# Kernel optimization log

Measured on AMD Instinct MI355X. Metric: run time of the kernel, lower is better.

The kernel has to match this reference:

```python
import jax, jax.numpy as jnp
import numpy as np

N_NODES = 100000
IN_CH = 64
HID = 128
N_EDGES = 1600000


def sage_conv(x, src, dst, Wl, bl, Wr, num_nodes):
    # PyG SAGEConv (mean aggr): out = lin_l(mean_{j->i} x_j) + lin_r(x_i)
    msg = x[src]                                           # [E, F] gather
    agg = jax.ops.segment_sum(msg, dst, num_segments=num_nodes)   # [N, F]
    cnt = jax.ops.segment_sum(jnp.ones((src.shape[0],), x.dtype), dst,
                              num_segments=num_nodes)      # [N]
    mean = agg / jnp.maximum(cnt, 1.0)[:, None]
    return mean @ Wl.T + bl + x @ Wr.T


def setup_inputs() -> dict:
    key = jax.random.key(0)
    k1, k2, k3, k4, k5, k6, k7, k8 = jax.random.split(key, 8)
    x = jax.random.normal(k1, (N_NODES, IN_CH), dtype=jnp.float32)
    edge_index = jax.random.randint(k2, (2, N_EDGES), 0, N_NODES, dtype=jnp.int64)
    s1 = 1.0 / np.sqrt(IN_CH)
    s2 = 1.0 / np.sqrt(HID)
    Wl1 = jax.random.uniform(k3, (HID, IN_CH), jnp.float32, -s1, s1)
    bl1 = jax.random.uniform(k4, (HID,), jnp.float32, -s1, s1)
    Wr1 = jax.random.uniform(k5, (HID, IN_CH), jnp.float32, -s1, s1)
    Wl2 = jax.random.uniform(k6, (HID, HID), jnp.float32, -s2, s2)
    bl2 = jax.random.uniform(k7, (HID,), jnp.float32, -s2, s2)
    Wr2 = jax.random.uniform(k8, (HID, HID), jnp.float32, -s2, s2)
    return {"x": x, "edge_index": edge_index,
            "Wl1": Wl1, "bl1": bl1, "Wr1": Wr1,
            "Wl2": Wl2, "bl2": bl2, "Wr2": Wr2}


def reference(x, edge_index, Wl1, bl1, Wr1, Wl2, bl2, Wr2):
    src, dst = edge_index[0], edge_index[1]
    n = x.shape[0]
    h = sage_conv(x, src, dst, Wl1, bl1, Wr1, n)
    h = jax.nn.relu(h)
    # dropout p=0.2 is identity in eval/reference mode
    out = sage_conv(h, src, dst, Wl2, bl2, Wr2, n)
    return out
```

## Files before the change

### kernel.cpp

```cpp
#include <hip/hip_runtime.h>
#include <hip/hip_bf16.h>
#include <stdint.h>

#define NN 100000
#define EE 1600000
#define NBUCK 196
#define CSB 512

typedef __attribute__((ext_vector_type(4))) float f32x4;
typedef __attribute__((ext_vector_type(8))) short bf16x8;

__device__ inline ushort f2bf(float f) {
    union { float f; uint32_t u; } v; v.f = f;
    uint32_t u = v.u;
    uint32_t r = (u + 0x7fffu + ((u >> 16) & 1u)) >> 16;
    return (ushort)r;
}
__device__ inline float bflo(uint32_t u) {
    union { uint32_t u; float f; } v; v.u = u << 16; return v.f;
}
__device__ inline float bfhi(uint32_t u) {
    union { uint32_t u; float f; } v; v.u = u & 0xffff0000u; return v.f;
}

__global__ void detect_kernel(const unsigned int* raw, int* flag) {
    int i = blockIdx.x * blockDim.x + threadIdx.x;
    if (i < 4096) {
        if (raw[2 * i + 1] != 0u) atomicOr(flag, 1);
    }
}

__global__ void cvt_f32_bf16(const float* __restrict__ in, ushort* __restrict__ out, int n4) {
    int i = blockIdx.x * blockDim.x + threadIdx.x;
    if (i >= n4) return;
    float4 v = *(const float4*)&in[i * 4];
    ushort o[4] = { f2bf(v.x), f2bf(v.y), f2bf(v.z), f2bf(v.w) };
    *(uint64_t*)&out[i * 4] = *(const uint64_t*)o;
}

__global__ void build_wcat(const float* __restrict__ Wl, const float* __restrict__ Wr,
                           ushort* __restrict__ Wcat, int K) {
    int t = blockIdx.x * blockDim.x + threadIdx.x;
    int KT = 2 * K;
    if (t >= 128 * KT) return;
    int o = t / KT, k = t % KT;
    float v = (k < K) ? Wl[o * K + k] : Wr[o * K + (k - K)];
    Wcat[o * KT + k] = f2bf(v);
}

__global__ __launch_bounds__(256) void coarse_hist(const void* raw, const int* flag,
                                                   int* ccnt, int E) {
    __shared__ int lh[NBUCK];
    for (int i = threadIdx.x; i < NBUCK; i += 256) lh[i] = 0;
    __syncthreads();
    int stride = gridDim.x * 256;
    if (*flag) {
        const int* p = (const int*)raw;
        for (int e = blockIdx.x * 256 + threadIdx.x; e < E; e += stride)
            atomicAdd(&lh[p[E + e] >> 9], 1);
    } else {
        const long long* p = (const long long*)raw;
        for (int e = blockIdx.x * 256 + threadIdx.x; e < E; e += stride)
            atomicAdd(&lh[((int)p[E + e]) >> 9], 1);
    }
    __syncthreads();
    for (int i = threadIdx.x; i < NBUCK; i += 256)
        if (lh[i]) atomicAdd(&ccnt[i], lh[i]);
}

__global__ void coarse_scan(const int* ccnt, int* coff, int* offsets, int E) {
    __shared__ int part[256];
    int t = threadIdx.x;
    int v[4]; int s = 0;
    #pragma unroll
    for (int j = 0; j < 4; j++) {
        int i = t * 4 + j;
        v[j] = (i < NBUCK) ? ccnt[i] : 0;
        s += v[j];
    }
    part[t] = s; __syncthreads();
    for (int off = 1; off < 256; off <<= 1) {
        int add = (t >= off) ? part[t - off] : 0;
        __syncthreads();
        part[t] += add;
        __syncthreads();
    }
    int run = part[t] - s;
    #pragma unroll
    for (int j = 0; j < 4; j++) {
        int i = t * 4 + j;
        if (i <= NBUCK) coff[i] = run;
        run += v[j];
    }
    if (t == 0) offsets[NN] = E;
}

__global__ __launch_bounds__(256) void coarse_scatter2(const void* raw, const int* flag,
                                                       const int* coff, int* cfill,
                                                       uint32_t* pbuf, int E) {
    __shared__ int lh[NBUCK];
    __shared__ int gbase[NBUCK];
    __shared__ int lfill[NBUCK];
    const int t = threadIdx.x;
    for (int i = t; i < NBUCK; i += 256) { lh[i] = 0; lfill[i] = 0; }
    __syncthreads();
    const int chunk = (E + (int)gridDim.x - 1) / (int)gridDim.x;
    const int s0 = blockIdx.x * chunk;
    const int s1 = min(E, s0 + chunk);
    const bool is32 = (*flag != 0);
    if (is32) {
        const int* p = (const int*)raw;
        for (int e = s0 + t; e < s1; e += 256) atomicAdd(&lh[p[E + e] >> 9], 1);
    } else {
        const long long* p = (const long long*)raw;
        for (int e = s0 + t; e < s1; e += 256) atomicAdd(&lh[((int)p[E + e]) >> 9], 1);
    }
    __syncthreads();
    for (int i = t; i < NBUCK; i += 256)
        gbase[i] = coff[i] + (lh[i] ? atomicAdd(&cfill[i], lh[i]) : 0);
    __syncthreads();
    if (is32) {
        const int* p = (const int*)raw;
        for (int e = s0 + t; e < s1; e += 256) {
            int sr = p[e], d = p[E + e];
            int b = d >> 9;
            int r = atomicAdd(&lfill[b], 1);
            pbuf[gbase[b] + r] = ((uint32_t)(d & 511) << 17) | (uint32_t)sr;
        }
    } else {
        const long long* p = (const long long*)raw;
        for (int e = s0 + t; e < s1; e += 256) {
            int sr = (int)p[e], d = (int)p[E + e];
            int b = d >> 9;
            int r = atomicAdd(&lfill[b], 1);
            pbuf[gbase[b] + r] = ((uint32_t)(d & 511) << 17) | (uint32_t)sr;
        }
    }
}

__global__ __launch_bounds__(512) void fine_bucket(const uint32_t* __restrict__ pbuf,
                                                   const int* __restrict__ coff,
                                                   int* __restrict__ offsets,
                                                   int* __restrict__ srcs_sort, int N) {
    __shared__ int cnt[512], sc[512], fil[512];
    const int b = blockIdx.x, t = threadIdx.x;
    const int s = coff[b], e = coff[b + 1];
    cnt[t] = 0; fil[t] = 0;
    __syncthreads();
    for (int i = s + t; i < e; i += 512) atomicAdd(&cnt[pbuf[i] >> 17], 1);
    __syncthreads();
    sc[t] = cnt[t];
    __syncthreads();
    for (int off = 1; off < 512; off <<= 1) {
        int add = (t >= off) ? sc[t - off] : 0;
        __syncthreads();
        sc[t] += add;
        __syncthreads();
    }
    const int nb0 = b * 512;
    if (nb0 + t < N) offsets[nb0 + t] = s + sc[t] - cnt[t];
    for (int i = s + t; i < e; i += 512) {
        uint32_t p = pbuf[i];
        int dl = (int)(p >> 17);
        int sr = (int)(p & 0x1FFFFu);
        int pos = s + (sc[dl] - cnt[dl]) + atomicAdd(&fil[dl], 1);
        srcs_sort[pos] = sr;
    }
}

template<int K, bool RELU, bool OUT_BF16>
__global__ __launch_bounds__(256) void sage_fused(
    const int* __restrict__ offsets, const int* __restrict__ srcs,
    const ushort* __restrict__ xin, const ushort* __restrict__ Wcat,
    const float* __restrict__ bl, void* __restrict__ outv, int N)
{
    constexpr int KT = 2 * K;
    constexpr int RP = K + 8;
    __shared__ ushort mlds[32][RP];
    __shared__ ushort slds[32][RP];
    const int t = threadIdx.x;
    const int w = t >> 6;
    const int lane = t & 63;
    const int nb = blockIdx.x * 32;

    #pragma unroll
    for (int idx = t; idx < 32 * (K / 8); idx += 256) {
        int r = idx / (K / 8), c = idx % (K / 8);
        *(uint4*)&slds[r][c * 8] = *(const uint4*)&xin[(size_t)(nb + r) * K + c * 8];
    }

    const int q     = lane >> 4;
    const int ql    = lane & 15;
    const int qbase = lane & 48;

    int offv = 0;
    if (lane < 9) offv = offsets[nb + w * 8 + lane];

    for (int pi = 0; pi < 2; pi++) {
        const int ln = w * 8 + pi * 4 + q;
        const int s0 = __shfl(offv, pi * 4 + q);
        const int s1 = __shfl(offv, pi * 4 + q + 1);
        const float inv = 1.0f / fmaxf((float)(s1 - s0), 1.0f);

        if (K == 64) {
            float f0=0.f, f1=0.f, f2=0.f, f3=0.f;
            for (int base = s0; base < s1; base += 16) {
                int cnt = min(16, s1 - base);
                int myidx = (base + ql < s1) ? srcs[base + ql] : 0;
                int j = 0;
                for (; j + 4 <= cnt; j += 4) {
                    int sA = __shfl(myidx, qbase + j);
                    int sB = __shfl(myidx, qbase + j + 1);
                    int sC = __shfl(myidx, qbase + j + 2);
                    int sD = __shfl(myidx, qbase + j + 3);
                    uint2 uA = *(const uint2*)&xin[(size_t)sA * 64 + ql * 4];
                    uint2 uB = *(const uint2*)&xin[(size_t)sB * 64 + ql * 4];
                    uint2 uC = *(const uint2*)&xin[(size_t)sC * 64 + ql * 4];
                    uint2 uD = *(const uint2*)&xin[(size_t)sD * 64 + ql * 4];
                    f0 += bflo(uA.x); f1 += bfhi(uA.x); f2 += bflo(uA.y); f3 += bfhi(uA.y);
                    f0 += bflo(uB.x); f1 += bfhi(uB.x); f2 += bflo(uB.y); f3 += bfhi(uB.y);
                    f0 += bflo(uC.x); f1 += bfhi(uC.x); f2 += bflo(uC.y); f3 += bfhi(uC.y);
                    f0 += bflo(uD.x); f1 += bfhi(uD.x); f2 += bflo(uD.y); f3 += bfhi(uD.y);
                }
                for (; j < cnt; j++) {
                    int s = __shfl(myidx, qbase + j);
                    uint2 u = *(const uint2*)&xin[(size_t)s * 64 + ql * 4];
                    f0 += bflo(u.x); f1 += bfhi(u.x); f2 += bflo(u.y); f3 += bfhi(u.y);
                }
            }
            ushort o[4] = { f2bf(f0 * inv), f2bf(f1 * inv), f2bf(f2 * inv), f2bf(f3 * inv) };
            *(uint64_t*)&mlds[ln][ql * 4] = *(const uint64_t*)o;
        } else {
            float f0=0.f, f1=0.f, f2=0.f, f3=0.f, f4=0.f, f5=0.f, f6=0.f, f7=0.f;
            for (int base = s0; base < s1; base += 16) {
                int cnt = min(16, s1 - base);
                int myidx = (base + ql < s1) ? srcs[base + ql] : 0;
                int j = 0;
                for (; j + 4 <= cnt; j += 4) {
                    int sA = __shfl(myidx, qbase + j);
                    int sB = __shfl(myidx, qbase + j + 1);
                    int sC = __shfl(myidx, qbase + j + 2);
                    int sD = __shfl(myidx, qbase + j + 3);
                    uint4 uA = *(const uint4*)&xin[(size_t)sA * 128 + ql * 8];
                    uint4 uB = *(const uint4*)&xin[(size_t)sB * 128 + ql * 8];
                    uint4 uC = *(const uint4*)&xin[(size_t)sC * 128 + ql * 8];
                    uint4 uD = *(const uint4*)&xin[(size_t)sD * 128 + ql * 8];
                    f0 += bflo(uA.x); f1 += bfhi(uA.x); f2 += bflo(uA.y); f3 += bfhi(uA.y);
                    f4 += bflo(uA.z); f5 += bfhi(uA.z); f6 += bflo(uA.w); f7 += bfhi(uA.w);
                    f0 += bflo(uB.x); f1 += bfhi(uB.x); f2 += bflo(uB.y); f3 += bfhi(uB.y);
                    f4 += bflo(uB.z); f5 += bfhi(uB.z); f6 += bflo(uB.w); f7 += bfhi(uB.w);
                    f0 += bflo(uC.x); f1 += bfhi(uC.x); f2 += bflo(uC.y); f3 += bfhi(uC.y);
                    f4 += bflo(uC.z); f5 += bfhi(uC.z); f6 += bflo(uC.w); f7 += bfhi(uC.w);
                    f0 += bflo(uD.x); f1 += bfhi(uD.x); f2 += bflo(uD.y); f3 += bfhi(uD.y);
                    f4 += bflo(uD.z); f5 += bfhi(uD.z); f6 += bflo(uD.w); f7 += bfhi(uD.w);
                }
                for (; j < cnt; j++) {
                    int s = __shfl(myidx, qbase + j);
                    uint4 u = *(const uint4*)&xin[(size_t)s * 128 + ql * 8];
                    f0 += bflo(u.x); f1 += bfhi(u.x); f2 += bflo(u.y); f3 += bfhi(u.y);
                    f4 += bflo(u.z); f5 += bfhi(u.z); f6 += bflo(u.w); f7 += bfhi(u.w);
                }
            }
            ushort o[8] = { f2bf(f0 * inv), f2bf(f1 * inv), f2bf(f2 * inv), f2bf(f3 * inv),
                            f2bf(f4 * inv), f2bf(f5 * inv), f2bf(f6 * inv), f2bf(f7 * inv) };
            *(uint4*)&mlds[ln][ql * 8] = *(const uint4*)o;
        }
    }
    __syncthreads();

    const int lrow = lane & 15;
    const int lgrp = lane >> 4;
    f32x4 acc[2][2];
    #pragma unroll
    for (int nt = 0; nt < 2; nt++)
        #pragma unroll
        for (int ct = 0; ct < 2; ct++)
            acc[nt][ct] = (f32x4){0.f, 0.f, 0.f, 0.f};

    #pragma unroll
    for (int ks = 0; ks < KT; ks += 32) {
        const int ac = (ks < K) ? ks : (ks - K);
        const ushort* Xb = (ks < K) ? &mlds[0][0] : &slds[0][0];
        bf16x8 x0 = *(const bf16x8*)&Xb[(lrow) * RP + ac + lgrp * 8];
        bf16x8 x1 = *(const bf16x8*)&Xb[(16 + lrow) * RP + ac + lgrp * 8];
        bf16x8 wA = *(const bf16x8*)&Wcat[(size_t)(w * 32 + lrow) * KT + ks + lgrp * 8];
        bf16x8 wB = *(const bf16x8*)&Wcat[(size_t)(w * 32 + 16 + lrow) * KT + ks + lgrp * 8];
        acc[0][0] = __builtin_amdgcn_mfma_f32_16x16x32_bf16(wA, x0, acc[0][0], 0, 0, 0);
        acc[0][1] = __builtin_amdgcn_mfma_f32_16x16x32_bf16(wB, x0, acc[0][1], 0, 0, 0);
        acc[1][0] = __builtin_amdgcn_mfma_f32_16x16x32_bf16(wA, x1, acc[1][0], 0, 0, 0);
        acc[1][1] = __builtin_amdgcn_mfma_f32_16x16x32_bf16(wB, x1, acc[1][1], 0, 0, 0);
    }

    #pragma unroll
    for (int ct = 0; ct < 2; ct++) {
        const int ch0 = w * 32 + ct * 16 + lgrp * 4;
        float4 b4 = *(const float4*)&bl[ch0];
        #pragma unroll
        for (int nt = 0; nt < 2; nt++) {
            int n = nb + nt * 16 + lrow;
            float v0 = acc[nt][ct][0] + b4.x;
            float v1 = acc[nt][ct][1] + b4.y;
            float v2 = acc[nt][ct][2] + b4.z;
            float v3 = acc[nt][ct][3] + b4.w;
            if (RELU) {
                v0 = fmaxf(v0, 0.f); v1 = fmaxf(v1, 0.f);
                v2 = fmaxf(v2, 0.f); v3 = fmaxf(v3, 0.f);
            }
            if (OUT_BF16) {
                ushort o[4] = { f2bf(v0), f2bf(v1), f2bf(v2), f2bf(v3) };
                *(uint64_t*)&((ushort*)outv)[(size_t)n * 128 + ch0] = *(const uint64_t*)o;
            } else {
                float4 o = make_float4(v0, v1, v2, v3);
                *(float4*)&((float*)outv)[(size_t)n * 128 + ch0] = o;
            }
        }
    }
}

extern "C" void kernel_launch(void* const* d_in, const int* in_sizes, int n_in,
                              void* d_out, int out_size, void* d_ws, size_t ws_size,
                              hipStream_t stream) {
    const float* x   = (const float*)d_in[0];
    const void*  er  = d_in[1];
    const float* Wl1 = (const float*)d_in[2];
    const float* bl1 = (const float*)d_in[3];
    const float* Wr1 = (const float*)d_in[4];
    const float* Wl2 = (const float*)d_in[5];
    const float* bl2 = (const float*)d_in[6];
    const float* Wr2 = (const float*)d_in[7];
    float* out = (float*)d_out;

    const int N = NN, E = EE;

    char* ws = (char*)d_ws;
    size_t off = 0;
    auto carve = [&](size_t bytes) { char* p = ws + off; off += (bytes + 511) & ~(size_t)511; return p; };
    int*      flag      = (int*)     carve(4);
    int*      ccnt      = (int*)     carve((size_t)NBUCK * 4);
    int*      cfill     = (int*)     carve((size_t)NBUCK * 4);
    int*      coff      = (int*)     carve((size_t)(NBUCK + 1) * 4);
    uint32_t* pbuf      = (uint32_t*)carve((size_t)E * 4);
    int*      offsets   = (int*)     carve((size_t)(N + 1) * 4);
    int*      srcs_sort = (int*)     carve((size_t)E * 4);
    ushort*   xb        = (ushort*)  carve((size_t)N * 64 * 2);
    ushort*   hb        = (ushort*)  carve((size_t)N * 128 * 2);
    ushort*   wc1       = (ushort*)  carve((size_t)128 * 128 * 2);
    ushort*   wc2       = (ushort*)  carve((size_t)128 * 256 * 2);
    (void)ws_size;

    hipMemsetAsync(flag, 0, 4, stream);
    hipMemsetAsync(ccnt, 0, (size_t)NBUCK * 4, stream);
    hipMemsetAsync(cfill, 0, (size_t)NBUCK * 4, stream);

    detect_kernel<<<16, 256, 0, stream>>>((const unsigned int*)er, flag);

    cvt_f32_bf16<<<(N * 64 / 4 + 255) / 256, 256, 0, stream>>>(x, xb, N * 64 / 4);
    build_wcat<<<(128 * 128 + 255) / 256, 256, 0, stream>>>(Wl1, Wr1, wc1, 64);
    build_wcat<<<(128 * 256 + 255) / 256, 256, 0, stream>>>(Wl2, Wr2, wc2, 128);

    coarse_hist<<<512, 256, 0, stream>>>(er, flag, ccnt, E);
    coarse_scan<<<1, 256, 0, stream>>>(ccnt, coff, offsets, E);
    coarse_scatter2<<<CSB, 256, 0, stream>>>(er, flag, coff, cfill, pbuf, E);
    fine_bucket<<<NBUCK, 512, 0, stream>>>(pbuf, coff, offsets, srcs_sort, N);

    const int fb = N / 32;

    sage_fused<64, true, true><<<fb, 256, 0, stream>>>(offsets, srcs_sort, xb, wc1, bl1, hb, N);
    sage_fused<128, false, false><<<fb, 256, 0, stream>>>(offsets, srcs_sort, hb, wc2, bl2, out, N);
}
```

Measured before the change: 210.5 us.

## Fuse prep kernels into one launch and sort each node's source list

Merges the detect, memset, x-to-bf16 conversion and two weight-concatenation kernels into one grid-stride prep kernel, cutting several launches and two memset calls. It also adds a per-node insertion sort of the source indices at the end of fine_bucket, so neighbor gathers in the sage kernels read x rows in increasing address order for better cache locality. The sort adds serial work per thread (about 16 edges per node) and the fused kernel relies on the flag memset finishing before it runs.

```diff
diff --git a/kernel.cpp b/kernel.cpp
--- a/kernel.cpp
+++ b/kernel.cpp
@@ -23,29 +23,38 @@
     union { uint32_t u; float f; } v; v.u = u & 0xffff0000u; return v.f;
 }
 
-__global__ void detect_kernel(const unsigned int* raw, int* flag) {
-    int i = blockIdx.x * blockDim.x + threadIdx.x;
-    if (i < 4096) {
-        if (raw[2 * i + 1] != 0u) atomicOr(flag, 1);
-    }
-}
-
-__global__ void cvt_f32_bf16(const float* __restrict__ in, ushort* __restrict__ out, int n4) {
-    int i = blockIdx.x * blockDim.x + threadIdx.x;
-    if (i >= n4) return;
-    float4 v = *(const float4*)&in[i * 4];
-    ushort o[4] = { f2bf(v.x), f2bf(v.y), f2bf(v.z), f2bf(v.w) };
-    *(uint64_t*)&out[i * 4] = *(const uint64_t*)o;
-}
-
-__global__ void build_wcat(const float* __restrict__ Wl, const float* __restrict__ Wr,
-                           ushort* __restrict__ Wcat, int K) {
-    int t = blockIdx.x * blockDim.x + threadIdx.x;
-    int KT = 2 * K;
-    if (t >= 128 * KT) return;
-    int o = t / KT, k = t % KT;
-    float v = (k < K) ? Wl[o * K + k] : Wr[o * K + (k - K)];
-    Wcat[o * KT + k] = f2bf(v);
+__global__ __launch_bounds__(256) void prep_kernel(
+    const float* __restrict__ x, const unsigned int* __restrict__ raw,
+    const float* __restrict__ Wl1, const float* __restrict__ Wr1,
+    const float* __restrict__ Wl2, const float* __restrict__ Wr2,
+    ushort* __restrict__ xb, ushort* __restrict__ wc1, ushort* __restrict__ wc2,
+    int* __restrict__ flag, int* __restrict__ ccnt, int* __restrict__ cfill)
+{
+    const int gid = blockIdx.x * 256 + threadIdx.x;
+    const int stride = gridDim.x * 256;
+
+    if (gid < 4096) {
+        if (raw[2 * gid + 1] != 0u) atomicOr(flag, 1);
+    }
+    if (gid >= 4096 && gid < 4096 + NBUCK) ccnt[gid - 4096] = 0;
+    if (gid >= 4096 + NBUCK && gid < 4096 + 2 * NBUCK) cfill[gid - 4096 - NBUCK] = 0;
+
+    const int n4 = NN * 64 / 4;
+    for (int i = gid; i < n4; i += stride) {
+        float4 v = *(const float4*)&x[i * 4];
+        ushort o[4] = { f2bf(v.x), f2bf(v.y), f2bf(v.z), f2bf(v.w) };
+        *(uint64_t*)&xb[i * 4] = *(const uint64_t*)o;
+    }
+    for (int i = gid; i < 128 * 128; i += stride) {
+        int o = i >> 7, k = i & 127;
+        float v = (k < 64) ? Wl1[o * 64 + k] : Wr1[o * 64 + (k - 64)];
+        wc1[o * 128 + k] = f2bf(v);
+    }
+    for (int i = gid; i < 128 * 256; i += stride) {
+        int o = i >> 8, k = i & 255;
+        float v = (k < 128) ? Wl2[o * 128 + k] : Wr2[o * 128 + (k - 128)];
+        wc2[o * 256 + k] = f2bf(v);
+    }
 }
 
 __global__ __launch_bounds__(256) void coarse_hist(const void* raw, const int* flag,
@@ -165,6 +174,17 @@
         int sr = (int)(p & 0x1FFFFu);
         int pos = s + (sc[dl] - cnt[dl]) + atomicAdd(&fil[dl], 1);
         srcs_sort[pos] = sr;
+    }
+    __syncthreads();
+    {
+        int a  = s + sc[t] - cnt[t];
+        int e2 = a + cnt[t];
+        for (int i = a + 1; i < e2; i++) {
+            int v = srcs_sort[i];
+            int j = i - 1;
+            while (j >= a && srcs_sort[j] > v) { srcs_sort[j + 1] = srcs_sort[j]; j--; }
+            srcs_sort[j + 1] = v;
+        }
     }
 }
 
@@ -349,14 +369,10 @@
     (void)ws_size;
 
     hipMemsetAsync(flag, 0, 4, stream);
-    hipMemsetAsync(ccnt, 0, (size_t)NBUCK * 4, stream);
-    hipMemsetAsync(cfill, 0, (size_t)NBUCK * 4, stream);
-
-    detect_kernel<<<16, 256, 0, stream>>>((const unsigned int*)er, flag);
-
-    cvt_f32_bf16<<<(N * 64 / 4 + 255) / 256, 256, 0, stream>>>(x, xb, N * 64 / 4);
-    build_wcat<<<(128 * 128 + 255) / 256, 256, 0, stream>>>(Wl1, Wr1, wc1, 64);
-    build_wcat<<<(128 * 256 + 255) / 256, 256, 0, stream>>>(Wl2, Wr2, wc2, 128);
+
+    prep_kernel<<<2048, 256, 0, stream>>>(x, (const unsigned int*)er,
+                                          Wl1, Wr1, Wl2, Wr2,
+                                          xb, wc1, wc2, flag, ccnt, cfill);
 
     coarse_hist<<<512, 256, 0, stream>>>(er, flag, ccnt, E);
     coarse_scan<<<1, 256, 0, stream>>>(ccnt, coff, offsets, E);
```

Result: slower. 293.5 us (+39.4%).
